# Kernel optimization log

Measured on AMD Instinct MI355X. Metric: run time of the kernel, lower is better.

The kernel has to match this reference:

```python
import jax, jax.numpy as jnp
import numpy as np

BANDWITH = 10.0  # matches init kwarg `bandwith`


def setup_inputs() -> dict:
    key = jax.random.key(0)
    kx, ky = jax.random.split(key)
    X = jax.random.normal(kx, (8192, 128), dtype=jnp.float32)
    Y = jax.random.normal(ky, (8192, 128), dtype=jnp.float32)
    return {"X": X, "Y": Y}


def reference(X, Y):
    # Z = vstack([X, Y]) : [N+M, d]
    Z = jnp.concatenate([X, Y], axis=0)
    # squared euclidean cdist: ||zi||^2 + ||zj||^2 - 2 zi.zj  (clamped >= 0)
    sq = jnp.sum(Z * Z, axis=-1)  # [N+M]
    d2 = sq[:, None] + sq[None, :] - 2.0 * jnp.matmul(Z, Z.T)
    d2 = jnp.maximum(d2, 0.0)
    # RBF kernel; the original's [None,...].sum(dim=0) over a single bandwidth is identity
    K = jnp.exp(-d2 / (2.0 * BANDWITH ** 2))  # [N+M, N+M]
    n = X.shape[0]
    XX = jnp.mean(K[:n, :n])
    XY = jnp.mean(K[:n, n:])
    YY = jnp.mean(K[n:, n:])
    return XX - 2.0 * XY + YY
```

## Files before the change

### kernel.cpp

```cpp
#include <hip/hip_runtime.h>
#include <math.h>

#define TD 128
#define BT 64
#define TB 256

typedef _Float16 half8 __attribute__((ext_vector_type(8)));
typedef _Float16 half2v __attribute__((ext_vector_type(2)));
typedef float f32x4 __attribute__((ext_vector_type(4)));

#define C2f   (-0.0072134752044448f)
#define M2C2f (0.0144269504088896f)

#if __has_builtin(__builtin_amdgcn_exp2f)
#define EXP2F(x) __builtin_amdgcn_exp2f(x)
#else
#define EXP2F(x) exp2f(x)
#endif

__device__ __forceinline__ void gload16(const void* g, void* l) {
    __builtin_amdgcn_global_load_lds(
        (const __attribute__((address_space(1))) void*)g,
        (__attribute__((address_space(3))) void*)l, 16, 0, 0);
}

#define LDS_B   65536
#define LDS_EA  131072
#define LDS_EB  132096
#define LDS_RED 133120

__global__ __launch_bounds__(256) void cvt_norms_kernel(const float* __restrict__ X,
                                                        const float* __restrict__ Y,
                                                        int n, int tot,
                                                        _Float16* __restrict__ Z16,
                                                        float* __restrict__ En) {
    const int wid  = (blockIdx.x * 256 + threadIdx.x) >> 6;
    const int lane = threadIdx.x & 63;
    if (wid >= tot) return;
    const float* row = (wid < n) ? (X + (size_t)wid * TD) : (Y + (size_t)(wid - n) * TD);
    float2 v = *reinterpret_cast<const float2*>(row + lane * 2);
    _Float16 hx = (_Float16)v.x;
    _Float16 hy = (_Float16)v.y;
    half2v h2 = {hx, hy};
    *reinterpret_cast<half2v*>(Z16 + (size_t)wid * TD + lane * 2) = h2;
    float fx = (float)hx, fy = (float)hy;
    float s = fmaf(fx, fx, fy * fy);
#pragma unroll
    for (int off = 32; off > 0; off >>= 1) s += __shfl_down(s, off, 64);
    if (lane == 0) En[wid] = EXP2F(C2f * s);
}

__global__ __launch_bounds__(512, 2) void mmd_mfma_kernel(const _Float16* __restrict__ Z16,
                                                          const float* __restrict__ En,
                                                          double* __restrict__ partials,
                                                          int n, int m, int T) {
    __shared__ char sAB[133152];

    const int t = blockIdx.x;
    double bguess = (2.0 * T + 1.0 -
                     sqrt((2.0 * T + 1.0) * (2.0 * T + 1.0) - 8.0 * (double)t)) * 0.5;
    int bi = (int)bguess;
    if (bi < 0) bi = 0;
    if (bi > T - 1) bi = T - 1;
    while ((bi + 1) * T - ((bi + 1) * bi) / 2 <= t) ++bi;
    while (bi * T - (bi * (bi - 1)) / 2 > t) --bi;
    const int bj = bi + (t - (bi * T - (bi * (bi - 1)) / 2));

    const int tid = threadIdx.x;
    const int l = tid & 63;
    const int w = tid >> 6;

    {
        const _Float16* gA = Z16 + (size_t)bi * TB * TD;
        const _Float16* gB = Z16 + (size_t)bj * TB * TD;
        const int rl = l >> 4;
        const int sl = l & 15;
#pragma unroll
        for (int c = 0; c < 8; ++c) {
            const int ci = c * 8 + w;
            const int r  = ci * 4 + rl;
            const int src = sl ^ (r & 15);
            gload16(gA + (size_t)r * TD + src * 8, sAB + ci * 1024);
            gload16(gB + (size_t)r * TD + src * 8, sAB + LDS_B + ci * 1024);
        }
        if (w == 0) gload16(En + bi * TB + l * 4, sAB + LDS_EA);
        if (w == 1) gload16(En + bj * TB + l * 4, sAB + LDS_EB);
    }
    __syncthreads();

    const int wrow = (w >> 2) * 128;
    const int wcol = (w & 3) * 64;
    const int lr = l & 15;
    const int kq = l >> 4;

    const char* pA = sAB;
    const char* pB = sAB + LDS_B;

    f32x4 acc[8][4];
    const f32x4 zero4 = {0.f, 0.f, 0.f, 0.f};

    {
        half8 bf[4];
#pragma unroll
        for (int j = 0; j < 4; ++j) {
            const int slot = kq ^ lr;
            bf[j] = *reinterpret_cast<const half8*>(pB + (wcol + j * 16 + lr) * 256 + slot * 16);
        }
#pragma unroll
        for (int i = 0; i < 8; ++i) {
            const int slot = kq ^ lr;
            half8 af = *reinterpret_cast<const half8*>(pA + (wrow + i * 16 + lr) * 256 + slot * 16);
#pragma unroll
            for (int j = 0; j < 4; ++j)
                acc[i][j] = __builtin_amdgcn_mfma_f32_16x16x32_f16(af, bf[j], zero4, 0, 0, 0);
        }
    }
#pragma unroll
    for (int ks = 1; ks < 4; ++ks) {
        half8 bf[4];
        const int slot = (ks * 4 + kq) ^ lr;
#pragma unroll
        for (int j = 0; j < 4; ++j)
            bf[j] = *reinterpret_cast<const half8*>(pB + (wcol + j * 16 + lr) * 256 + slot * 16);
#pragma unroll
        for (int i = 0; i < 8; ++i) {
            half8 af = *reinterpret_cast<const half8*>(pA + (wrow + i * 16 + lr) * 256 + slot * 16);
#pragma unroll
            for (int j = 0; j < 4; ++j)
                acc[i][j] = __builtin_amdgcn_mfma_f32_16x16x32_f16(af, bf[j], acc[i][j], 0, 0, 0);
        }
    }

    float Ej[4];
#pragma unroll
    for (int j = 0; j < 4; ++j)
        Ej[j] = *reinterpret_cast<const float*>(sAB + LDS_EB + (wcol + j * 16 + lr) * 4);
    f32x4 EiV[8];
#pragma unroll
    for (int i = 0; i < 8; ++i)
        EiV[i] = *reinterpret_cast<const f32x4*>(sAB + LDS_EA + (wrow + i * 16 + kq * 4) * 4);

    float s = 0.f;
#pragma unroll
    for (int j = 0; j < 4; ++j) {
        float sj0 = 0.f, sj1 = 0.f;
#pragma unroll
        for (int i = 0; i < 8; ++i) {
#pragma unroll
            for (int r = 0; r < 4; ++r) {
                float e = EXP2F(M2C2f * acc[i][j][r]);
                if (r & 1) sj1 = fmaf(EiV[i][r], e, sj1);
                else       sj0 = fmaf(EiV[i][r], e, sj0);
            }
        }
        s = fmaf(Ej[j], sj0 + sj1, s);
    }

#pragma unroll
    for (int off = 32; off > 0; off >>= 1) s += __shfl_down(s, off, 64);
    float* sred = reinterpret_cast<float*>(sAB + LDS_RED);
    if (l == 0) sred[w] = s;
    __syncthreads();
    if (tid == 0) {
        float bs = 0.f;
#pragma unroll
        for (int q = 0; q < 8; ++q) bs += sred[q];
        double wa = (bi * TB < n) ? (1.0 / (double)n) : (-1.0 / (double)m);
        double wb = (bj * TB < n) ? (1.0 / (double)n) : (-1.0 / (double)m);
        double wgt = wa * wb * ((bi == bj) ? 1.0 : 2.0);
        partials[t] = wgt * (double)bs;
    }
}

__global__ __launch_bounds__(256) void norms_kernel(const float* __restrict__ X,
                                                    const float* __restrict__ Y,
                                                    int n, int tot,
                                                    float* __restrict__ norms) {
    int r = blockIdx.x * 256 + threadIdx.x;
    if (r >= tot) return;
    const float* row = (r < n) ? (X + (size_t)r * TD) : (Y + (size_t)(r - n) * TD);
    float s = 0.f;
#pragma unroll
    for (int k = 0; k < TD; k += 4) {
        float4 v = *reinterpret_cast<const float4*>(row + k);
        s = fmaf(v.x, v.x, s); s = fmaf(v.y, v.y, s);
        s = fmaf(v.z, v.z, s); s = fmaf(v.w, v.w, s);
    }
    norms[r] = s;
}

__global__ __launch_bounds__(256, 2) void mmd_tile_kernel(const float* __restrict__ X,
                                                          const float* __restrict__ Y,
                                                          const float* __restrict__ norms,
                                                          double* __restrict__ partials,
                                                          int n, int m, int T) {
    __shared__ float sA[TD][BT];
    __shared__ float sB[TD][BT];
    __shared__ float sredf[4];

    const int t = blockIdx.x;
    double bguess = (2.0 * T + 1.0 -
                     sqrt((2.0 * T + 1.0) * (2.0 * T + 1.0) - 8.0 * (double)t)) * 0.5;
    int bi = (int)bguess;
    if (bi < 0) bi = 0;
    if (bi > T - 1) bi = T - 1;
    while ((bi + 1) * T - ((bi + 1) * bi) / 2 <= t) ++bi;
    while (bi * T - (bi * (bi - 1)) / 2 > t) --bi;
    const int bj = bi + (t - (bi * T - (bi * (bi - 1)) / 2));

    const int tid = threadIdx.x;
    {
        const int row = tid & 63;
        const int qb  = tid >> 6;
        const int ra = bi * BT + row;
        const int rb = bj * BT + row;
        const float* Arow = (ra < n) ? (X + (size_t)ra * TD) : (Y + (size_t)(ra - n) * TD);
        const float* Brow = (rb < n) ? (X + (size_t)rb * TD) : (Y + (size_t)(rb - n) * TD);
#pragma unroll
        for (int i = 0; i < 8; ++i) {
            const int q = qb + 4 * i;
            float4 va = *reinterpret_cast<const float4*>(Arow + 4 * q);
            sA[4 * q + 0][row] = va.x; sA[4 * q + 1][row] = va.y;
            sA[4 * q + 2][row] = va.z; sA[4 * q + 3][row] = va.w;
            float4 vb = *reinterpret_cast<const float4*>(Brow + 4 * q);
            sB[4 * q + 0][row] = vb.x; sB[4 * q + 1][row] = vb.y;
            sB[4 * q + 2][row] = vb.z; sB[4 * q + 3][row] = vb.w;
        }
    }
    __syncthreads();

    const int tx = tid & 15;
    const int ty = tid >> 4;
    float acc[4][4];
#pragma unroll
    for (int i = 0; i < 4; ++i)
#pragma unroll
        for (int j = 0; j < 4; ++j) acc[i][j] = 0.f;

#pragma unroll 16
    for (int k = 0; k < TD; ++k) {
        float4 a = *reinterpret_cast<const float4*>(&sA[k][ty * 4]);
        float4 b = *reinterpret_cast<const float4*>(&sB[k][tx * 4]);
        const float av[4] = {a.x, a.y, a.z, a.w};
        const float bv[4] = {b.x, b.y, b.z, b.w};
#pragma unroll
        for (int i = 0; i < 4; ++i)
#pragma unroll
            for (int j = 0; j < 4; ++j)
                acc[i][j] = fmaf(av[i], bv[j], acc[i][j]);
    }

    float nA[4], nB[4];
#pragma unroll
    for (int i = 0; i < 4; ++i) nA[i] = norms[bi * BT + ty * 4 + i];
#pragma unroll
    for (int j = 0; j < 4; ++j) nB[j] = norms[bj * BT + tx * 4 + j];

    const float cexp = -0.005f;
    float s = 0.f;
#pragma unroll
    for (int i = 0; i < 4; ++i)
#pragma unroll
        for (int j = 0; j < 4; ++j) {
            float d2 = fmaxf(nA[i] + nB[j] - 2.f * acc[i][j], 0.f);
            s += __expf(d2 * cexp);
        }

#pragma unroll
    for (int off = 32; off > 0; off >>= 1) s += __shfl_down(s, off, 64);
    if ((tid & 63) == 0) sredf[tid >> 6] = s;
    __syncthreads();
    if (tid == 0) {
        double wa = (bi * BT < n) ? (1.0 / (double)n) : (-1.0 / (double)m);
        double wb = (bj * BT < n) ? (1.0 / (double)n) : (-1.0 / (double)m);
        double wgt = wa * wb * ((bi == bj) ? 1.0 : 2.0);
        partials[t] = wgt * (double)(sredf[0] + sredf[1] + sredf[2] + sredf[3]);
    }
}

__global__ __launch_bounds__(256) void reduce_kernel(const double* __restrict__ partials,
                                                     int npart,
                                                     float* __restrict__ out) {
    __shared__ double sd[256];
    double s = 0.0;
    for (int i = threadIdx.x; i < npart; i += 256) s += partials[i];
    sd[threadIdx.x] = s;
    __syncthreads();
    for (int off = 128; off > 0; off >>= 1) {
        if ((int)threadIdx.x < off) sd[threadIdx.x] += sd[threadIdx.x + off];
        __syncthreads();
    }
    if (threadIdx.x == 0) out[0] = (float)sd[0];
}

extern "C" void kernel_launch(void* const* d_in, const int* in_sizes, int n_in,
                              void* d_out, int out_size, void* d_ws, size_t ws_size,
                              hipStream_t stream) {
    const float* X = (const float*)d_in[0];
    const float* Y = (const float*)d_in[1];
    float* out = (float*)d_out;

    const int n = in_sizes[0] / TD;
    const int m = in_sizes[1] / TD;
    const int tot = n + m;

    const size_t z16_bytes = (size_t)tot * TD * 2;
    const size_t en_off    = (z16_bytes + 255) & ~(size_t)255;
    const size_t en_bytes  = (size_t)tot * 4;
    const size_t part_off  = ((en_off + en_bytes) + 255) & ~(size_t)255;
    const int Tm = tot / TB;
    const int npart_m = Tm * (Tm + 1) / 2;
    const size_t needed = part_off + (size_t)npart_m * 8;

    if (ws_size >= needed && (tot % TB) == 0 && (n % TB) == 0) {
        _Float16* Z16 = (_Float16*)d_ws;
        float* En = (float*)((char*)d_ws + en_off);
        double* partials = (double*)((char*)d_ws + part_off);
        cvt_norms_kernel<<<(tot + 3) / 4, 256, 0, stream>>>(X, Y, n, tot, Z16, En);
        mmd_mfma_kernel<<<npart_m, 512, 0, stream>>>(Z16, En, partials, n, m, Tm);
        reduce_kernel<<<1, 256, 0, stream>>>(partials, npart_m, out);
    } else {
        const int T = tot / BT;
        const int npart = T * (T + 1) / 2;
        float* norms = (float*)d_ws;
        double* partials = (double*)((char*)d_ws + (((size_t)tot * 4 + 255) & ~(size_t)255));
        norms_kernel<<<(tot + 255) / 256, 256, 0, stream>>>(X, Y, n, tot, norms);
        mmd_tile_kernel<<<npart, 256, 0, stream>>>(X, Y, norms, partials, n, m, T);
        reduce_kernel<<<1, 256, 0, stream>>>(partials, npart, out);
    }
}
```

Measured before the change: 68.90 us.

## Make MFMA MMD kernel persistent with K-split double-buffered tile prefetch

Replaces the one-tile-per-block MFMA kernel with a persistent kernel of 256 blocks that loops over triangular tiles. Each tile's K dimension is split into two halves held in separate LDS buffers, so the next tile's first half is loaded while the current second half is computed. Synchronisation uses manual vmcnt waits and raw barriers, and s_setprio raises priority around the MFMA sections. It aims to hide global-to-LDS load latency and cut block launch overhead. The hand-counted waitcnt values and a fixed grid of 256 add risk of races and of load imbalance across the 528 tiles.

After: 67.14 us. 2.6% less time.

```diff
diff --git a/kernel.cpp b/kernel.cpp
--- a/kernel.cpp
+++ b/kernel.cpp
@@ -4,6 +4,7 @@
 #define TD 128
 #define BT 64
 #define TB 256
+#define GRID 256
 
 typedef _Float16 half8 __attribute__((ext_vector_type(8)));
 typedef _Float16 half2v __attribute__((ext_vector_type(2)));
@@ -18,16 +19,35 @@
 #define EXP2F(x) exp2f(x)
 #endif
 
+#define LA0 0
+#define LA1 32768
+#define LB0 65536
+#define LB1 98304
+#define LEA 131072
+#define LEB 132096
+#define LRED 133120
+#define LDS_TOT 133152
+
+#define FENCE() asm volatile("" ::: "memory")
+#define SCHEDB() __builtin_amdgcn_sched_barrier(0)
+
 __device__ __forceinline__ void gload16(const void* g, void* l) {
     __builtin_amdgcn_global_load_lds(
         (const __attribute__((address_space(1))) void*)g,
         (__attribute__((address_space(3))) void*)l, 16, 0, 0);
 }
 
-#define LDS_B   65536
-#define LDS_EA  131072
-#define LDS_EB  132096
-#define LDS_RED 133120
+__device__ __forceinline__ void decode_tile(int t, int T, int& bi, int& bj) {
+    double bguess = (2.0 * T + 1.0 -
+                     sqrt((2.0 * T + 1.0) * (2.0 * T + 1.0) - 8.0 * (double)t)) * 0.5;
+    int b = (int)bguess;
+    if (b < 0) b = 0;
+    if (b > T - 1) b = T - 1;
+    while ((b + 1) * T - ((b + 1) * b) / 2 <= t) ++b;
+    while (b * T - (b * (b - 1)) / 2 > t) --b;
+    bi = b;
+    bj = b + (t - (b * T - (b * (b - 1)) / 2));
+}
 
 __global__ __launch_bounds__(256) void cvt_norms_kernel(const float* __restrict__ X,
                                                         const float* __restrict__ Y,
@@ -50,125 +70,172 @@
     if (lane == 0) En[wid] = EXP2F(C2f * s);
 }
 
-__global__ __launch_bounds__(512, 2) void mmd_mfma_kernel(const _Float16* __restrict__ Z16,
+__global__ __launch_bounds__(512, 2) void mmd_pipe_kernel(const _Float16* __restrict__ Z16,
                                                           const float* __restrict__ En,
                                                           double* __restrict__ partials,
-                                                          int n, int m, int T) {
-    __shared__ char sAB[133152];
-
-    const int t = blockIdx.x;
-    double bguess = (2.0 * T + 1.0 -
-                     sqrt((2.0 * T + 1.0) * (2.0 * T + 1.0) - 8.0 * (double)t)) * 0.5;
-    int bi = (int)bguess;
-    if (bi < 0) bi = 0;
-    if (bi > T - 1) bi = T - 1;
-    while ((bi + 1) * T - ((bi + 1) * bi) / 2 <= t) ++bi;
-    while (bi * T - (bi * (bi - 1)) / 2 > t) --bi;
-    const int bj = bi + (t - (bi * T - (bi * (bi - 1)) / 2));
+                                                          int n, int m, int T, int ntiles) {
+    __shared__ char lds[LDS_TOT];
 
     const int tid = threadIdx.x;
     const int l = tid & 63;
     const int w = tid >> 6;
-
-    {
-        const _Float16* gA = Z16 + (size_t)bi * TB * TD;
-        const _Float16* gB = Z16 + (size_t)bj * TB * TD;
-        const int rl = l >> 4;
-        const int sl = l & 15;
-#pragma unroll
-        for (int c = 0; c < 8; ++c) {
-            const int ci = c * 8 + w;
-            const int r  = ci * 4 + rl;
-            const int src = sl ^ (r & 15);
-            gload16(gA + (size_t)r * TD + src * 8, sAB + ci * 1024);
-            gload16(gB + (size_t)r * TD + src * 8, sAB + LDS_B + ci * 1024);
-        }
-        if (w == 0) gload16(En + bi * TB + l * 4, sAB + LDS_EA);
-        if (w == 1) gload16(En + bj * TB + l * 4, sAB + LDS_EB);
-    }
-    __syncthreads();
-
     const int wrow = (w >> 2) * 128;
     const int wcol = (w & 3) * 64;
     const int lr = l & 15;
     const int kq = l >> 4;
-
-    const char* pA = sAB;
-    const char* pB = sAB + LDS_B;
-
-    f32x4 acc[8][4];
-    const f32x4 zero4 = {0.f, 0.f, 0.f, 0.f};
+    const int swz = lr & 7;
+
+    const int rsub = l >> 3;
+    const int psl  = l & 7;
+    const int srcsw = (psl ^ rsub) << 4;
+
+    int it = blockIdx.x;
+    if (it >= ntiles) return;
+
+    int bi, bj;
+    decode_tile(it, T, bi, bj);
 
     {
-        half8 bf[4];
+        const char* gA = (const char*)(Z16 + (size_t)bi * TB * TD);
+        const char* gB = (const char*)(Z16 + (size_t)bj * TB * TD);
+#pragma unroll
+        for (int q = 0; q < 4; ++q) {
+            const int chunk = w * 4 + q;
+            const int row = chunk * 8 + rsub;
+            gload16(gA + (size_t)row * 256 + srcsw, lds + LA0 + chunk * 1024);
+            gload16(gB + (size_t)row * 256 + srcsw, lds + LB0 + chunk * 1024);
+        }
+    }
+
+    while (true) {
+        {
+            const char* gA = (const char*)(Z16 + (size_t)bi * TB * TD);
+            const char* gB = (const char*)(Z16 + (size_t)bj * TB * TD);
+#pragma unroll
+            for (int q = 0; q < 4; ++q) {
+                const int chunk = w * 4 + q;
+                const int row = chunk * 8 + rsub;
+                gload16(gA + (size_t)row * 256 + 128 + srcsw, lds + LA1 + chunk * 1024);
+                gload16(gB + (size_t)row * 256 + 128 + srcsw, lds + LB1 + chunk * 1024);
+            }
+            if (w == 0) gload16(En + (size_t)bi * TB + l * 4, lds + LEA);
+            if (w == 1) gload16(En + (size_t)bj * TB + l * 4, lds + LEB);
+        }
+        if (w < 2) asm volatile("s_waitcnt vmcnt(9)" ::: "memory");
+        else       asm volatile("s_waitcnt vmcnt(8)" ::: "memory");
+        SCHEDB();
+        __builtin_amdgcn_s_barrier();
+        SCHEDB();
+
+        f32x4 acc[8][4];
+        const f32x4 zero4 = {0.f, 0.f, 0.f, 0.f};
+        __builtin_amdgcn_s_setprio(1);
+#pragma unroll
+        for (int kk = 0; kk < 2; ++kk) {
+            const int soff = ((kk * 4 + kq) ^ swz) << 4;
+            half8 bf[4];
+#pragma unroll
+            for (int j = 0; j < 4; ++j)
+                bf[j] = *reinterpret_cast<const half8*>(lds + LB0 + (wcol + j * 16 + lr) * 128 + soff);
+#pragma unroll
+            for (int i = 0; i < 8; ++i) {
+                half8 af = *reinterpret_cast<const half8*>(lds + LA0 + (wrow + i * 16 + lr) * 128 + soff);
+#pragma unroll
+                for (int j = 0; j < 4; ++j)
+                    acc[i][j] = __builtin_amdgcn_mfma_f32_16x16x32_f16(
+                        af, bf[j], (kk == 0) ? zero4 : acc[i][j], 0, 0, 0);
+            }
+        }
+        __builtin_amdgcn_s_setprio(0);
+
+        FENCE();
+        __builtin_amdgcn_s_barrier();
+        SCHEDB();
+
+        const int itn = it + GRID;
+        const bool more = (itn < ntiles);
+        int bin = bi, bjn = bj;
+        if (more) {
+            decode_tile(itn, T, bin, bjn);
+            const char* gA = (const char*)(Z16 + (size_t)bin * TB * TD);
+            const char* gB = (const char*)(Z16 + (size_t)bjn * TB * TD);
+#pragma unroll
+            for (int q = 0; q < 4; ++q) {
+                const int chunk = w * 4 + q;
+                const int row = chunk * 8 + rsub;
+                gload16(gA + (size_t)row * 256 + srcsw, lds + LA0 + chunk * 1024);
+                gload16(gB + (size_t)row * 256 + srcsw, lds + LB0 + chunk * 1024);
+            }
+        }
+        if (more) asm volatile("s_waitcnt vmcnt(8)" ::: "memory");
+        else      asm volatile("s_waitcnt vmcnt(0)" ::: "memory");
+        SCHEDB();
+        __builtin_amdgcn_s_barrier();
+        SCHEDB();
+
+        __builtin_amdgcn_s_setprio(1);
+#pragma unroll
+        for (int kk = 0; kk < 2; ++kk) {
+            const int soff = ((kk * 4 + kq) ^ swz) << 4;
+            half8 bf[4];
+#pragma unroll
+            for (int j = 0; j < 4; ++j)
+                bf[j] = *reinterpret_cast<const half8*>(lds + LB1 + (wcol + j * 16 + lr) * 128 + soff);
+#pragma unroll
+            for (int i = 0; i < 8; ++i) {
+                half8 af = *reinterpret_cast<const half8*>(lds + LA1 + (wrow + i * 16 + lr) * 128 + soff);
+#pragma unroll
+                for (int j = 0; j < 4; ++j)
+                    acc[i][j] = __builtin_amdgcn_mfma_f32_16x16x32_f16(af, bf[j], acc[i][j], 0, 0, 0);
+            }
+        }
+        __builtin_amdgcn_s_setprio(0);
+
+        float Ej[4];
+#pragma unroll
+        for (int j = 0; j < 4; ++j)
+            Ej[j] = *reinterpret_cast<const float*>(lds + LEB + (wcol + j * 16 + lr) * 4);
+        f32x4 EiV[8];
+#pragma unroll
+        for (int i = 0; i < 8; ++i)
+            EiV[i] = *reinterpret_cast<const f32x4*>(lds + LEA + (wrow + i * 16 + kq * 4) * 4);
+
+        float s = 0.f;
 #pragma unroll
         for (int j = 0; j < 4; ++j) {
-            const int slot = kq ^ lr;
-            bf[j] = *reinterpret_cast<const half8*>(pB + (wcol + j * 16 + lr) * 256 + slot * 16);
-        }
-#pragma unroll
-        for (int i = 0; i < 8; ++i) {
-            const int slot = kq ^ lr;
-            half8 af = *reinterpret_cast<const half8*>(pA + (wrow + i * 16 + lr) * 256 + slot * 16);
-#pragma unroll
-            for (int j = 0; j < 4; ++j)
-                acc[i][j] = __builtin_amdgcn_mfma_f32_16x16x32_f16(af, bf[j], zero4, 0, 0, 0);
-        }
-    }
-#pragma unroll
-    for (int ks = 1; ks < 4; ++ks) {
-        half8 bf[4];
-        const int slot = (ks * 4 + kq) ^ lr;
-#pragma unroll
-        for (int j = 0; j < 4; ++j)
-            bf[j] = *reinterpret_cast<const half8*>(pB + (wcol + j * 16 + lr) * 256 + slot * 16);
-#pragma unroll
-        for (int i = 0; i < 8; ++i) {
-            half8 af = *reinterpret_cast<const half8*>(pA + (wrow + i * 16 + lr) * 256 + slot * 16);
-#pragma unroll
-            for (int j = 0; j < 4; ++j)
-                acc[i][j] = __builtin_amdgcn_mfma_f32_16x16x32_f16(af, bf[j], acc[i][j], 0, 0, 0);
-        }
-    }
-
-    float Ej[4];
-#pragma unroll
-    for (int j = 0; j < 4; ++j)
-        Ej[j] = *reinterpret_cast<const float*>(sAB + LDS_EB + (wcol + j * 16 + lr) * 4);
-    f32x4 EiV[8];
-#pragma unroll
-    for (int i = 0; i < 8; ++i)
-        EiV[i] = *reinterpret_cast<const f32x4*>(sAB + LDS_EA + (wrow + i * 16 + kq * 4) * 4);
-
-    float s = 0.f;
-#pragma unroll
-    for (int j = 0; j < 4; ++j) {
-        float sj0 = 0.f, sj1 = 0.f;
-#pragma unroll
-        for (int i = 0; i < 8; ++i) {
-#pragma unroll
-            for (int r = 0; r < 4; ++r) {
-                float e = EXP2F(M2C2f * acc[i][j][r]);
-                if (r & 1) sj1 = fmaf(EiV[i][r], e, sj1);
-                else       sj0 = fmaf(EiV[i][r], e, sj0);
-            }
-        }
-        s = fmaf(Ej[j], sj0 + sj1, s);
-    }
-
-#pragma unroll
-    for (int off = 32; off > 0; off >>= 1) s += __shfl_down(s, off, 64);
-    float* sred = reinterpret_cast<float*>(sAB + LDS_RED);
-    if (l == 0) sred[w] = s;
-    __syncthreads();
-    if (tid == 0) {
-        float bs = 0.f;
-#pragma unroll
-        for (int q = 0; q < 8; ++q) bs += sred[q];
-        double wa = (bi * TB < n) ? (1.0 / (double)n) : (-1.0 / (double)m);
-        double wb = (bj * TB < n) ? (1.0 / (double)n) : (-1.0 / (double)m);
-        double wgt = wa * wb * ((bi == bj) ? 1.0 : 2.0);
-        partials[t] = wgt * (double)bs;
+            float sj0 = 0.f, sj1 = 0.f;
+#pragma unroll
+            for (int i = 0; i < 8; ++i) {
+#pragma unroll
+                for (int r = 0; r < 4; ++r) {
+                    float e = EXP2F(M2C2f * acc[i][j][r]);
+                    if (r & 1) sj1 = fmaf(EiV[i][r], e, sj1);
+                    else       sj0 = fmaf(EiV[i][r], e, sj0);
+                }
+            }
+            s = fmaf(Ej[j], sj0 + sj1, s);
+        }
+
+#pragma unroll
+        for (int off = 32; off > 0; off >>= 1) s += __shfl_down(s, off, 64);
+        if (l == 0) *reinterpret_cast<float*>(lds + LRED + w * 4) = s;
+        asm volatile("s_waitcnt lgkmcnt(0)" ::: "memory");
+        SCHEDB();
+        __builtin_amdgcn_s_barrier();
+        SCHEDB();
+        if (tid == 0) {
+            const float* sred = reinterpret_cast<const float*>(lds + LRED);
+            float bs = 0.f;
+#pragma unroll
+            for (int q = 0; q < 8; ++q) bs += sred[q];
+            double wa = (bi * TB < n) ? (1.0 / (double)n) : (-1.0 / (double)m);
+            double wb = (bj * TB < n) ? (1.0 / (double)n) : (-1.0 / (double)m);
+            double wgt = wa * wb * ((bi == bj) ? 1.0 : 2.0);
+            partials[it] = wgt * (double)bs;
+        }
+
+        if (!more) break;
+        it = itn; bi = bin; bj = bjn;
     }
 }
 
@@ -199,14 +266,8 @@
     __shared__ float sredf[4];
 
     const int t = blockIdx.x;
-    double bguess = (2.0 * T + 1.0 -
-                     sqrt((2.0 * T + 1.0) * (2.0 * T + 1.0) - 8.0 * (double)t)) * 0.5;
-    int bi = (int)bguess;
-    if (bi < 0) bi = 0;
-    if (bi > T - 1) bi = T - 1;
-    while ((bi + 1) * T - ((bi + 1) * bi) / 2 <= t) ++bi;
-    while (bi * T - (bi * (bi - 1)) / 2 > t) --bi;
-    const int bj = bi + (t - (bi * T - (bi * (bi - 1)) / 2));
+    int bi, bj;
+    decode_tile(t, T, bi, bj);
 
     const int tid = threadIdx.x;
     {
@@ -317,7 +378,8 @@
         float* En = (float*)((char*)d_ws + en_off);
         double* partials = (double*)((char*)d_ws + part_off);
         cvt_norms_kernel<<<(tot + 3) / 4, 256, 0, stream>>>(X, Y, n, tot, Z16, En);
-        mmd_mfma_kernel<<<npart_m, 512, 0, stream>>>(Z16, En, partials, n, m, Tm);
+        int grid = (npart_m < GRID) ? npart_m : GRID;
+        mmd_pipe_kernel<<<grid, 512, 0, stream>>>(Z16, En, partials, n, m, Tm, npart_m);
         reduce_kernel<<<1, 256, 0, stream>>>(partials, npart_m, out);
     } else {
         const int T = tot / BT;
```
